# Performance work log

Hardware: AMD Instinct MI355X
Metric: run time of the kernel (lower is better)

Reference implementation:

```python
import jax, jax.numpy as jnp
import numpy as np

ALIBI_SLOPES = jnp.array([0.6299605249, 0.396850263, 0.25, 0.1574901312,
                          0.0992125657, 0.0625, 0.0393725328, 0.0248031414,
                          0.015625, 0.0098431332, 0.0062007854, 0.00390625],
                         dtype=jnp.float32)
H, D = 12, 64
SCALE = D ** (-0.5)


def setup_inputs() -> dict:
    key = jax.random.key(0)
    ks = jax.random.split(key, 9)
    B, S, E = 4, 2048, 768
    s = 0.02
    return {
        "x": jax.random.normal(ks[0], (B, S, E), dtype=jnp.float32),
        "Wq": jax.random.normal(ks[1], (E, E), dtype=jnp.float32) * s,
        "bq": jnp.zeros((E,), dtype=jnp.float32),
        "Wk": jax.random.normal(ks[2], (E, E), dtype=jnp.float32) * s,
        "bk": jnp.zeros((E,), dtype=jnp.float32),
        "Wv": jax.random.normal(ks[3], (E, E), dtype=jnp.float32) * s,
        "bv": jnp.zeros((E,), dtype=jnp.float32),
        "Wo": jax.random.normal(ks[4], (E, E), dtype=jnp.float32) * s,
        "bo": jnp.zeros((E,), dtype=jnp.float32),
    }


def reference(x, Wq, bq, Wk, bk, Wv, bv, Wo, bo):
    B, S, E = x.shape
    # projections (weights stored input-major: y = x @ W + b)
    q = (x @ Wq + bq).reshape(B, S, H, D).transpose(0, 2, 1, 3)  # [B,H,S,D]
    k = (x @ Wk + bk).reshape(B, S, H, D).transpose(0, 2, 1, 3)
    v = (x @ Wv + bv).reshape(B, S, H, D).transpose(0, 2, 1, 3)

    scores = jnp.einsum('bhqd,bhkd->bhqk', q, k) * SCALE  # [B,H,S,S]

    pos = jnp.arange(S, dtype=jnp.float32)
    a = ALIBI_SLOPES[:, None] * pos[None, :]          # [H,S]
    alibi = a[:, :, None] - a[:, None, :]             # [H,S,S]
    scores = scores + alibi[None]

    causal = jnp.triu(jnp.ones((S, S), dtype=bool), k=1)  # True above diag
    scores = jnp.where(causal[None, None], -jnp.inf, scores)

    attn = jax.nn.softmax(scores, axis=-1)
    o = jnp.einsum('bhqk,bhkd->bhqd', attn, v)  # [B,H,S,D]

    # Faithful to original: view of contiguous (B,H,S,D) buffer as (B,S,E)
    # (head-major flatten, reproducing the original module's reshape).
    o = o.reshape(B, S, E)
    return o @ Wo + bo
```

## Files before the change

### kernel.cpp

```cpp
#include <hip/hip_runtime.h>
#include <hip/hip_bf16.h>
#include <cstdint>
#include <cstddef>

#define B_ 4
#define S_ 2048
#define E_ 768
#define H_ 12
#define D_ 64

typedef __bf16 bf16x8 __attribute__((ext_vector_type(8)));
typedef float f32x4 __attribute__((ext_vector_type(4)));

__constant__ float c_slopes[12] = {
    0.6299605249f, 0.396850263f, 0.25f, 0.1574901312f,
    0.0992125657f, 0.0625f, 0.0393725328f, 0.0248031414f,
    0.015625f, 0.0098431332f, 0.0062007854f, 0.00390625f};

__device__ __forceinline__ unsigned short f2bf_u(float f) {
    unsigned u = __builtin_bit_cast(unsigned, f);
    u += 0x7fffu + ((u >> 16) & 1u);
    return (unsigned short)(u >> 16);
}
__device__ __forceinline__ __bf16 f2bf(float f) {
    unsigned short s = f2bf_u(f);
    return __builtin_bit_cast(__bf16, s);
}

__device__ __forceinline__ void gload_lds16(const void* g, void* l) {
    __builtin_amdgcn_global_load_lds(
        (const __attribute__((address_space(1))) unsigned int*)g,
        (__attribute__((address_space(3))) unsigned int*)l, 16, 0, 0);
}

__global__ __launch_bounds__(256) void prep(
    const float* __restrict__ x, __bf16* __restrict__ xb,
    const float* __restrict__ W0, const float* __restrict__ W1,
    const float* __restrict__ W2, const float* __restrict__ W3,
    __bf16* __restrict__ Wt) {
    __shared__ alignas(16) __bf16 ts[64 * 72];
    const int L = blockIdx.x;
    const int t = threadIdx.x;
    if (L < 6144) {
        int i = (L * 256 + t) * 4;
        float4 v = *(const float4*)(x + i);
        ushort4 o;
        o.x = f2bf_u(v.x); o.y = f2bf_u(v.y); o.z = f2bf_u(v.z); o.w = f2bf_u(v.w);
        *(ushort4*)((unsigned short*)xb + i) = o;
        return;
    }
    const int id = L - 6144;
    const int z = id / 144, rem = id % 144;
    const int k0 = (rem / 12) * 64, n0 = (rem % 12) * 64;
    const float* W = z == 0 ? W0 : z == 1 ? W1 : z == 2 ? W2 : W3;
    __bf16* out = Wt + (size_t)z * E_ * E_;
#pragma unroll
    for (int i = 0; i < 4; i++) {
        int idx = i * 256 + t;
        int row = idx >> 4, c4 = idx & 15;
        float4 v = *(const float4*)(W + (size_t)(k0 + row) * E_ + n0 + c4 * 4);
        ts[(c4 * 4 + 0) * 72 + row] = f2bf(v.x);
        ts[(c4 * 4 + 1) * 72 + row] = f2bf(v.y);
        ts[(c4 * 4 + 2) * 72 + row] = f2bf(v.z);
        ts[(c4 * 4 + 3) * 72 + row] = f2bf(v.w);
    }
    __syncthreads();
#pragma unroll
    for (int i = 0; i < 2; i++) {
        int idx = i * 256 + t;
        int r = idx >> 3, c8 = idx & 7;
        *(uint4*)((unsigned short*)out + (size_t)(n0 + r) * E_ + k0 + c8 * 8) =
            *(const uint4*)((const unsigned short*)ts + r * 72 + c8 * 8);
    }
}

__global__ __launch_bounds__(256, 3) void qkv_gemm(
    const __bf16* __restrict__ A, const __bf16* __restrict__ WtAll,
    const float* __restrict__ b0, const float* __restrict__ b1,
    const float* __restrict__ b2, __bf16* __restrict__ Qb,
    __bf16* __restrict__ Kb, __bf16* __restrict__ Vtb) {
    constexpr int Kd = E_;
    __shared__ alignas(16) __bf16 Asm[2][128 * 32];
    __shared__ alignas(16) __bf16 Bsm[2][3][64 * 32];

    const int t = threadIdx.x;
    const int w = t >> 6, lane = t & 63;
    const int qm = lane & 15, quad = lane >> 4;
    const int m0 = blockIdx.y * 128, n0 = blockIdx.x * 64;
    const int wm = w * 32;

    float bvv[3][4];
    const float* bs[3] = {b0, b1, b2};
#pragma unroll
    for (int z = 0; z < 3; z++)
#pragma unroll
        for (int j = 0; j < 4; j++) bvv[z][j] = bs[z][n0 + j * 16 + qm];

    const int crow = lane >> 2;
    const int scol = (lane & 3) ^ ((lane >> 3) & 3);
    const int cq = (quad ^ ((qm >> 1) & 3)) * 8;

    f32x4 acc[3][2][4] = {};

    for (int k0 = 0; k0 < Kd; k0 += 64) {
#pragma unroll
        for (int p = 0; p < 2; p++) {
            const int kp = k0 + p * 32;
#pragma unroll
            for (int cc = 0; cc < 2; cc++) {
                int chunk = w * 2 + cc;
                gload_lds16((const unsigned short*)A +
                                (size_t)(m0 + chunk * 16 + crow) * Kd + kp + scol * 8,
                            Asm[p] + chunk * 512);
            }
#pragma unroll
            for (int e = 0; e < 3; e++) {
                int g = w * 3 + e;
                int z = g >> 2, cz = g & 3;
                gload_lds16((const unsigned short*)WtAll + (size_t)z * Kd * E_ +
                                (size_t)(n0 + cz * 16 + crow) * Kd + kp + scol * 8,
                            Bsm[p][z] + cz * 512);
            }
        }
        __syncthreads();

#pragma unroll
        for (int p = 0; p < 2; p++) {
            bf16x8 af[2];
#pragma unroll
            for (int i = 0; i < 2; i++)
                af[i] = *(const bf16x8*)(Asm[p] + (wm + i * 16 + qm) * 32 + cq);
#pragma unroll
            for (int z = 0; z < 3; z++) {
                bf16x8 bg[4];
#pragma unroll
                for (int j = 0; j < 4; j++)
                    bg[j] = *(const bf16x8*)(Bsm[p][z] + (j * 16 + qm) * 32 + cq);
#pragma unroll
                for (int i = 0; i < 2; i++)
#pragma unroll
                    for (int j = 0; j < 4; j++)
                        acc[z][i][j] = __builtin_amdgcn_mfma_f32_16x16x32_bf16(
                            af[i], bg[j], acc[z][i][j], 0, 0, 0);
            }
        }
        __syncthreads();
    }

#pragma unroll
    for (int z = 0; z < 3; z++) {
        __bf16* out = z == 0 ? Qb : z == 1 ? Kb : Vtb;
#pragma unroll
        for (int i = 0; i < 2; i++) {
#pragma unroll
            for (int j = 0; j < 4; j++) {
                int col = n0 + j * 16 + qm;
                int rowb = m0 + wm + i * 16 + quad * 4;
                int h = col >> 6, d = col & (D_ - 1);
                if (z == 2) {
                    int b = rowb >> 11, s = rowb & (S_ - 1);
                    unsigned short pk4[4];
#pragma unroll
                    for (int r = 0; r < 4; r++)
                        pk4[r] = f2bf_u(acc[z][i][j][r] + bvv[z][j]);
                    uint2 pv;
                    pv.x = (unsigned)pk4[0] | ((unsigned)pk4[1] << 16);
                    pv.y = (unsigned)pk4[2] | ((unsigned)pk4[3] << 16);
                    *(uint2*)((unsigned short*)out +
                              ((size_t)(b * H_ + h) * D_ + d) * S_ + s) = pv;
                } else {
#pragma unroll
                    for (int r = 0; r < 4; r++) {
                        int row = rowb + r;
                        int b = row >> 11, s = row & (S_ - 1);
                        out[(((size_t)(b * H_ + h)) * S_ + s) * D_ + d] =
                            f2bf(acc[z][i][j][r] + bvv[z][j]);
                    }
                }
            }
        }
    }
}

__global__ __launch_bounds__(256, 3) void gemm_out(
    const __bf16* __restrict__ A, const __bf16* __restrict__ Wt,
    const float* __restrict__ bias, float* __restrict__ outF) {
    constexpr int Kd = E_, N = E_;
    __shared__ alignas(16) __bf16 Asm[2][128 * 32];
    __shared__ alignas(16) __bf16 Bsm[2][64 * 32];

    const int t = threadIdx.x;
    const int w = t >> 6, lane = t & 63;
    const int qm = lane & 15, quad = lane >> 4;
    const int m0 = blockIdx.y * 128, n0 = blockIdx.x * 64;
    const int wm = w * 32;

    float bvv[4];
#pragma unroll
    for (int j = 0; j < 4; j++) bvv[j] = bias[n0 + j * 16 + qm];

    const int crow = lane >> 2;
    const int scol = (lane & 3) ^ ((lane >> 3) & 3);
    const int cq = (quad ^ ((qm >> 1) & 3)) * 8;

    f32x4 acc[2][4] = {};

    for (int k0 = 0; k0 < Kd; k0 += 64) {
#pragma unroll
        for (int p = 0; p < 2; p++) {
            const int kp = k0 + p * 32;
#pragma unroll
            for (int cc = 0; cc < 2; cc++) {
                int chunk = w * 2 + cc;
                gload_lds16((const unsigned short*)A +
                                (size_t)(m0 + chunk * 16 + crow) * Kd + kp + scol * 8,
                            Asm[p] + chunk * 512);
            }
            gload_lds16((const unsigned short*)Wt +
                            (size_t)(n0 + w * 16 + crow) * Kd + kp + scol * 8,
                        Bsm[p] + w * 512);
        }
        __syncthreads();

#pragma unroll
        for (int p = 0; p < 2; p++) {
            bf16x8 af[2], bg[4];
#pragma unroll
            for (int i = 0; i < 2; i++)
                af[i] = *(const bf16x8*)(Asm[p] + (wm + i * 16 + qm) * 32 + cq);
#pragma unroll
            for (int j = 0; j < 4; j++)
                bg[j] = *(const bf16x8*)(Bsm[p] + (j * 16 + qm) * 32 + cq);
#pragma unroll
            for (int i = 0; i < 2; i++)
#pragma unroll
                for (int j = 0; j < 4; j++)
                    acc[i][j] = __builtin_amdgcn_mfma_f32_16x16x32_bf16(
                        af[i], bg[j], acc[i][j], 0, 0, 0);
        }
        __syncthreads();
    }

#pragma unroll
    for (int i = 0; i < 2; i++) {
#pragma unroll
        for (int j = 0; j < 4; j++) {
            int col = n0 + j * 16 + qm;
            int rowb = m0 + wm + i * 16 + quad * 4;
#pragma unroll
            for (int r = 0; r < 4; r++)
                outF[(size_t)(rowb + r) * N + col] = acc[i][j][r] + bvv[j];
        }
    }
}

__global__ __launch_bounds__(256, 6) void attn_k(
    const __bf16* __restrict__ Q, const __bf16* __restrict__ K,
    const __bf16* __restrict__ Vt, __bf16* __restrict__ O) {
    __shared__ alignas(16) __bf16 Ksm[2][64 * 32];
    __shared__ alignas(16) __bf16 Vsm[2][64 * 32];
    __shared__ alignas(16) __bf16 Psm[4 * 16 * 64];

    const int t = threadIdx.x;
    const int w = t >> 6, lane = t & 63;
    const int qm = lane & 15, quad = lane >> 4;
    const int L = blockIdx.x;
    const int r = L & 7;
    const int m = (L >> 3) & 31;
    const int s = L >> 8;
    const int bh = r * 6 + s;
    const int qt = (m + s * 5 + (s >> 1)) & 31;
    const float c2 = c_slopes[bh % H_] * 1.44269504f;
    const size_t base = (size_t)bh * S_ * D_;

    const int bb = qt * 64 + w * 16;
    const __bf16* qp = Q + base + (size_t)(bb + qm) * D_ + quad * 8;
    bf16x8 qf0 = *(const bf16x8*)qp;
    bf16x8 qf1 = *(const bf16x8*)(qp + 32);

    f32x4 oacc[4] = {};
    float lsum = 0.f;
    char* Pb = (char*)Psm + w * 2048;

    const int srow = lane >> 2;
    const int sq = (lane & 3) ^ ((lane >> 3) & 3);
    const unsigned short* Kg = (const unsigned short*)K + base +
                               (size_t)(16 * w + srow) * D_ + sq * 8;
    const unsigned short* Vg = (const unsigned short*)Vt + base +
                               (size_t)(16 * w + srow) * S_ + sq * 8;

    const int cq = (quad ^ ((qm >> 1) & 3)) * 8;
    const int pf = (qm & 7) << 4;

    const float scl = 0.18033688f;
    float cst[4], crr[4];
#pragma unroll
    for (int i = 0; i < 4; i++) cst[i] = -c2 * (float)(16 * i + 4 * quad);
#pragma unroll
    for (int rr = 0; rr < 4; rr++) crr[rr] = -c2 * (float)rr;
    const int qi = bb + qm;

    auto body = [&](int kt, bool domask) {
#pragma unroll
        for (int h = 0; h < 2; h++) {
            gload_lds16(Kg + (size_t)(kt * 64) * D_ + 32 * h, Ksm[h] + w * 512);
            gload_lds16(Vg + kt * 64 + 32 * h, Vsm[h] + w * 512);
        }
        __syncthreads();

        bf16x8 ak[4][2], bv[4][2];
#pragma unroll
        for (int i = 0; i < 4; i++) {
            ak[i][0] = *(const bf16x8*)(Ksm[0] + (16 * i + qm) * 32 + cq);
            ak[i][1] = *(const bf16x8*)(Ksm[1] + (16 * i + qm) * 32 + cq);
        }
#pragma unroll
        for (int jd = 0; jd < 4; jd++) {
            bv[jd][0] = *(const bf16x8*)(Vsm[0] + (16 * jd + qm) * 32 + cq);
            bv[jd][1] = *(const bf16x8*)(Vsm[1] + (16 * jd + qm) * 32 + cq);
        }

        f32x4 st[4];
#pragma unroll
        for (int i = 0; i < 4; i++) {
            f32x4 zz = {0.f, 0.f, 0.f, 0.f};
            zz = __builtin_amdgcn_mfma_f32_16x16x32_bf16(ak[i][0], qf0, zz, 0, 0, 0);
            zz = __builtin_amdgcn_mfma_f32_16x16x32_bf16(ak[i][1], qf1, zz, 0, 0, 0);
            st[i] = zz;
        }

        const float kb = -c2 * (float)(kt * 64);
        float ls = 0.f;
        unsigned pk[4][2];
#pragma unroll
        for (int i = 0; i < 4; i++) {
            float bi = kb + cst[i];
            float p[4];
#pragma unroll
            for (int rr = 0; rr < 4; rr++) {
                float tt = st[i][rr] * scl + (bi + crr[rr]);
                float pp = __builtin_amdgcn_exp2f(tt);
                if (domask) {
                    int key = kt * 64 + 16 * i + 4 * quad + rr;
                    pp = (key > qi) ? 0.f : pp;
                }
                ls += pp;
                p[rr] = pp;
            }
            asm("v_cvt_pk_bf16_f32 %0, %1, %2"
                : "=v"(pk[i][0]) : "v"(p[0]), "v"(p[1]));
            asm("v_cvt_pk_bf16_f32 %0, %1, %2"
                : "=v"(pk[i][1]) : "v"(p[2]), "v"(p[3]));
        }
        lsum += ls;

#pragma unroll
        for (int i = 0; i < 4; i++) {
            uint2 pv; pv.x = pk[i][0]; pv.y = pk[i][1];
            *(uint2*)(Pb + qm * 128 + ((32 * i + 8 * quad) ^ pf)) = pv;
        }

        bf16x8 ap0 = *(const bf16x8*)(Pb + qm * 128 + ((quad * 16) ^ pf));
        bf16x8 ap1 = *(const bf16x8*)(Pb + qm * 128 + ((64 + quad * 16) ^ pf));
#pragma unroll
        for (int jd = 0; jd < 4; jd++) {
            oacc[jd] = __builtin_amdgcn_mfma_f32_16x16x32_bf16(
                ap0, bv[jd][0], oacc[jd], 0, 0, 0);
            oacc[jd] = __builtin_amdgcn_mfma_f32_16x16x32_bf16(
                ap1, bv[jd][1], oacc[jd], 0, 0, 0);
        }

        __syncthreads();
    };

    for (int kt = 0; kt < qt; kt++) body(kt, false);
    body(qt, true);

    float lf = lsum;
    lf += __shfl_xor(lf, 16);
    lf += __shfl_xor(lf, 32);
#pragma unroll
    for (int rr = 0; rr < 4; rr++) {
        float lr = __shfl(lf, 4 * quad + rr);
        float inv = 1.0f / lr;
        int qrow = bb + 4 * quad + rr;
#pragma unroll
        for (int jd = 0; jd < 4; jd++)
            O[base + (size_t)qrow * D_ + 16 * jd + qm] =
                f2bf(oacc[jd][rr] * inv);
    }
}

extern "C" void kernel_launch(void* const* d_in, const int* in_sizes, int n_in,
                              void* d_out, int out_size, void* d_ws, size_t ws_size,
                              hipStream_t stream) {
    (void)in_sizes; (void)n_in; (void)out_size; (void)ws_size;
    const float* x  = (const float*)d_in[0];
    const float* Wq = (const float*)d_in[1];
    const float* bq = (const float*)d_in[2];
    const float* Wk = (const float*)d_in[3];
    const float* bk = (const float*)d_in[4];
    const float* Wv = (const float*)d_in[5];
    const float* bv = (const float*)d_in[6];
    const float* Wo = (const float*)d_in[7];
    const float* bo = (const float*)d_in[8];
    float* out = (float*)d_out;

    const size_t n = (size_t)B_ * H_ * S_ * D_;
    __bf16* xb  = (__bf16*)d_ws;
    __bf16* Qb  = xb + n;
    __bf16* Kb  = xb + 2 * n;
    __bf16* Vtb = xb + 3 * n;
    __bf16* Wt  = xb + 4 * n;
    __bf16* Ob  = Qb;

    prep<<<6720, 256, 0, stream>>>(x, xb, Wq, Wk, Wv, Wo, Wt);
    qkv_gemm<<<dim3(12, 64), 256, 0, stream>>>(
        xb, Wt, bq, bk, bv, Qb, Kb, Vtb);
    attn_k<<<1536, 256, 0, stream>>>(Qb, Kb, Vtb, Ob);
    gemm_out<<<dim3(12, 64), 256, 0, stream>>>(
        Ob, Wt + 3 * (size_t)E_ * E_, bo, out);
}
```

Baseline: 208.7 us.

## Permute K rows so P stays in registers, dropping the LDS round trip

The K tile rows are now loaded from shared memory in a permuted order with a new swizzle. This makes the S=K·Q MFMA output layout line up with the A-operand layout needed for the P·V MFMA. The P matrix can then be packed straight from registers instead of being written to and read back from a per-wave shared buffer. This removes the LDS traffic for P and frees shared memory, which could raise occupancy. The cost is a more intricate index mapping, where a mismatch would silently corrupt the results.

```diff
diff --git a/kernel.cpp b/kernel.cpp
--- a/kernel.cpp
+++ b/kernel.cpp
@@ -11,6 +11,7 @@
 
 typedef __bf16 bf16x8 __attribute__((ext_vector_type(8)));
 typedef float f32x4 __attribute__((ext_vector_type(4)));
+typedef unsigned uint32x4 __attribute__((ext_vector_type(4)));
 
 __constant__ float c_slopes[12] = {
     0.6299605249f, 0.396850263f, 0.25f, 0.1574901312f,
@@ -259,7 +260,6 @@
     const __bf16* __restrict__ Vt, __bf16* __restrict__ O) {
     __shared__ alignas(16) __bf16 Ksm[2][64 * 32];
     __shared__ alignas(16) __bf16 Vsm[2][64 * 32];
-    __shared__ alignas(16) __bf16 Psm[4 * 16 * 64];
 
     const int t = threadIdx.x;
     const int w = t >> 6, lane = t & 63;
@@ -280,7 +280,6 @@
 
     f32x4 oacc[4] = {};
     float lsum = 0.f;
-    char* Pb = (char*)Psm + w * 2048;
 
     const int srow = lane >> 2;
     const int sq = (lane & 3) ^ ((lane >> 3) & 3);
@@ -289,13 +288,17 @@
     const unsigned short* Vg = (const unsigned short*)Vt + base +
                                (size_t)(16 * w + srow) * S_ + sq * 8;
 
-    const int cq = (quad ^ ((qm >> 1) & 3)) * 8;
-    const int pf = (qm & 7) << 4;
+    const int kbase = 8 * (qm >> 2) + (qm & 3);
+    const int cqa = (quad ^ ((qm >> 1) & 1)) * 8;
+    const int cqb = cqa ^ 16;
+    const int cqv = (quad ^ ((qm >> 1) & 3)) * 8;
+
+    const int o_i[4] = {0, 32, 4, 36};
 
     const float scl = 0.18033688f;
     float cst[4], crr[4];
 #pragma unroll
-    for (int i = 0; i < 4; i++) cst[i] = -c2 * (float)(16 * i + 4 * quad);
+    for (int i = 0; i < 4; i++) cst[i] = -c2 * (float)(8 * quad + o_i[i]);
 #pragma unroll
     for (int rr = 0; rr < 4; rr++) crr[rr] = -c2 * (float)rr;
     const int qi = bb + qm;
@@ -311,13 +314,15 @@
         bf16x8 ak[4][2], bv[4][2];
 #pragma unroll
         for (int i = 0; i < 4; i++) {
-            ak[i][0] = *(const bf16x8*)(Ksm[0] + (16 * i + qm) * 32 + cq);
-            ak[i][1] = *(const bf16x8*)(Ksm[1] + (16 * i + qm) * 32 + cq);
+            int row = kbase + o_i[i];
+            int cqk = (i < 2) ? cqa : cqb;
+            ak[i][0] = *(const bf16x8*)(Ksm[0] + row * 32 + cqk);
+            ak[i][1] = *(const bf16x8*)(Ksm[1] + row * 32 + cqk);
         }
 #pragma unroll
         for (int jd = 0; jd < 4; jd++) {
-            bv[jd][0] = *(const bf16x8*)(Vsm[0] + (16 * jd + qm) * 32 + cq);
-            bv[jd][1] = *(const bf16x8*)(Vsm[1] + (16 * jd + qm) * 32 + cq);
+            bv[jd][0] = *(const bf16x8*)(Vsm[0] + (16 * jd + qm) * 32 + cqv);
+            bv[jd][1] = *(const bf16x8*)(Vsm[1] + (16 * jd + qm) * 32 + cqv);
         }
 
         f32x4 st[4];
@@ -341,7 +346,7 @@
                 float tt = st[i][rr] * scl + (bi + crr[rr]);
                 float pp = __builtin_amdgcn_exp2f(tt);
                 if (domask) {
-                    int key = kt * 64 + 16 * i + 4 * quad + rr;
+                    int key = kt * 64 + 8 * quad + o_i[i] + rr;
                     pp = (key > qi) ? 0.f : pp;
                 }
                 ls += pp;
@@ -354,14 +359,10 @@
         }
         lsum += ls;
 
-#pragma unroll
-        for (int i = 0; i < 4; i++) {
-            uint2 pv; pv.x = pk[i][0]; pv.y = pk[i][1];
-            *(uint2*)(Pb + qm * 128 + ((32 * i + 8 * quad) ^ pf)) = pv;
-        }
-
-        bf16x8 ap0 = *(const bf16x8*)(Pb + qm * 128 + ((quad * 16) ^ pf));
-        bf16x8 ap1 = *(const bf16x8*)(Pb + qm * 128 + ((64 + quad * 16) ^ pf));
+        uint32x4 w0 = {pk[0][0], pk[0][1], pk[2][0], pk[2][1]};
+        uint32x4 w1 = {pk[1][0], pk[1][1], pk[3][0], pk[3][1]};
+        bf16x8 ap0 = __builtin_bit_cast(bf16x8, w0);
+        bf16x8 ap1 = __builtin_bit_cast(bf16x8, w1);
 #pragma unroll
         for (int jd = 0; jd < 4; jd++) {
             oacc[jd] = __builtin_amdgcn_mfma_f32_16x16x32_bf16(
```

Result: no change. 205.9 us (median of 2 runs) (-1.3%).
